# Kernel optimization log

Measured on AMD Instinct MI355X. Metric: run time of the kernel, lower is better.

The kernel has to match this reference:

```python
import jax, jax.numpy as jnp
import numpy as np

INPUT_DIM, HID_DIM, OUTPUT_DIM, N = 256, 128, 256, 16384
SCALE = 128 ** (-0.5)


def setup_inputs() -> dict:
    key = jax.random.key(0)
    ks = jax.random.split(key, 11)
    s_in = 1.0 / np.sqrt(INPUT_DIM)
    s_hid = 1.0 / np.sqrt(HID_DIM)
    return {
        "q": jax.random.normal(ks[0], (N, INPUT_DIM), jnp.float32),
        "k": jax.random.normal(ks[1], (N, INPUT_DIM), jnp.float32),
        "v": jax.random.normal(ks[2], (N, INPUT_DIM), jnp.float32),
        "Wq": jax.random.uniform(ks[3], (INPUT_DIM, HID_DIM), jnp.float32, -s_in, s_in),
        "bq": jax.random.uniform(ks[4], (HID_DIM,), jnp.float32, -s_in, s_in),
        "Wk": jax.random.uniform(ks[5], (INPUT_DIM, HID_DIM), jnp.float32, -s_in, s_in),
        "bk": jax.random.uniform(ks[6], (HID_DIM,), jnp.float32, -s_in, s_in),
        "Wv": jax.random.uniform(ks[7], (INPUT_DIM, HID_DIM), jnp.float32, -s_in, s_in),
        "bv": jax.random.uniform(ks[8], (HID_DIM,), jnp.float32, -s_in, s_in),
        "Wo": jax.random.uniform(ks[9], (HID_DIM, OUTPUT_DIM), jnp.float32, -s_hid, s_hid),
        "bo": jax.random.uniform(ks[10], (OUTPUT_DIM,), jnp.float32, -s_hid, s_hid),
    }


def reference(q, k, v, Wq, bq, Wk, bk, Wv, bv, Wo, bo):
    qh = q @ Wq + bq                      # [N, H]
    kh = k @ Wk + bk                      # [N, H]
    vh = v @ Wv + bv                      # [N, H]
    scores = (qh @ kh.T) * SCALE          # [N, N] materialized as in original
    attn = jax.nn.softmax(scores, axis=-1)
    out = attn @ vh                       # [N, H]
    return out @ Wo + bo                  # [N, OUTPUT_DIM]
```

## Files before the change

kernel.cpp:

```cpp
#include <hip/hip_runtime.h>
#include <hip/hip_bf16.h>
#include <stdint.h>


#define N_TOK 16384
#define IN_DIM 256
#define HID 128
#define OUT_DIM 256
#define KVB 32
#define BM 128
#define TOT_TILES (N_TOK / KVB)

typedef __bf16   bf16x8 __attribute__((ext_vector_type(8)));
typedef short    short8 __attribute__((ext_vector_type(8)));
typedef float    f32x4  __attribute__((ext_vector_type(4)));
typedef float    f32x16 __attribute__((ext_vector_type(16)));
typedef uint32_t u32x4  __attribute__((ext_vector_type(4)));

#define MFMA16(a,b,c) __builtin_amdgcn_mfma_f32_16x16x32_bf16((a),(b),(c),0,0,0)
#define MFMA32(a,b,c) __builtin_amdgcn_mfma_f32_32x32x16_bf16((a),(b),(c),0,0,0)
#define EXP2(x) __builtin_amdgcn_exp2f(x)

__device__ __forceinline__ short f2bf(float f) {
    union { float f; uint32_t u; } v; v.f = f;
    uint32_t r = v.u + 0x7FFFu + ((v.u >> 16) & 1u);
    return (short)(r >> 16);
}

__device__ __forceinline__ uint32_t cvtpk(float lo, float hi) {
    uint32_t d;
    asm("v_cvt_pk_bf16_f32 %0, %1, %2" : "=v"(d) : "v"(lo), "v"(hi));
    return d;
}

__device__ __forceinline__ void pswap(uint32_t& a, uint32_t& b) {
    auto r = __builtin_amdgcn_permlane32_swap(a, b, false, false);
    a = r[0]; b = r[1];
}

__device__ __forceinline__ void gl16(const void* g, const void* l) {
    __builtin_amdgcn_global_load_lds(
        (const __attribute__((address_space(1))) void*)g,
        (__attribute__((address_space(3))) void*)l, 16, 0, 0);
}

__global__ void wt4_kernel(const float* __restrict__ Wq, const float* __restrict__ Wk,
                           const float* __restrict__ Wv, const float* __restrict__ Wo,
                           short* __restrict__ tq, short* __restrict__ tk,
                           short* __restrict__ tv, short* __restrict__ to_)
{
    int idx = blockIdx.x * 256 + threadIdx.x;
    int w = idx >> 15, i = idx & 32767;
    if (w < 3) {
        const float* W = (w == 0) ? Wq : (w == 1) ? Wk : Wv;
        short* T = (w == 0) ? tq : (w == 1) ? tk : tv;
        int k = i >> 7, c = i & 127;
        T[c * 256 + k] = f2bf(W[i]);
    } else {
        int k = i >> 8, c = i & 255;
        to_[c * 128 + k] = f2bf(Wo[i]);
    }
}

__global__ __launch_bounds__(256) void proj3_kernel(
    const float* __restrict__ q, const float* __restrict__ k, const float* __restrict__ v,
    const short* __restrict__ tq, const short* __restrict__ tk, const short* __restrict__ tv,
    const float* __restrict__ bq, const float* __restrict__ bk, const float* __restrict__ bv,
    short* __restrict__ qh, short* __restrict__ kh, short* __restrict__ vh,
    float scale_q)
{
    const int y = blockIdx.y;
    const float* X  = (y == 0) ? q  : (y == 1) ? k  : v;
    const short* WT = (y == 0) ? tq : (y == 1) ? tk : tv;
    const float* bias = (y == 0) ? bq : (y == 1) ? bk : bv;
    short* Y = (y == 0) ? qh : (y == 1) ? kh : vh;
    const float post_scale = (y == 0) ? scale_q : 1.0f;

    const int lane = threadIdx.x & 63;
    const int wave = threadIdx.x >> 6;
    const int g = lane >> 4, c = lane & 15;
    const int rowbase = blockIdx.x * 64 + wave * 16;

    bf16x8 a[8];
    const float* xrow = X + (size_t)(rowbase + c) * IN_DIM;
#pragma unroll
    for (int kk = 0; kk < 8; ++kk) {
        const float* p = xrow + kk * 32 + 8 * g;
        float4 f0 = *(const float4*)(p);
        float4 f1 = *(const float4*)(p + 4);
        short8 t;
        t[0]=f2bf(f0.x); t[1]=f2bf(f0.y); t[2]=f2bf(f0.z); t[3]=f2bf(f0.w);
        t[4]=f2bf(f1.x); t[5]=f2bf(f1.y); t[6]=f2bf(f1.z); t[7]=f2bf(f1.w);
        a[kk] = __builtin_bit_cast(bf16x8, t);
    }

    f32x4 acc[8];
#pragma unroll
    for (int nf = 0; nf < 8; ++nf) acc[nf] = (f32x4){0.f, 0.f, 0.f, 0.f};

#pragma unroll
    for (int kk = 0; kk < 8; ++kk) {
#pragma unroll
        for (int nf = 0; nf < 8; ++nf) {
            bf16x8 b = *(const bf16x8*)(WT + (size_t)(c + 16 * nf) * IN_DIM + kk * 32 + 8 * g);
            acc[nf] = MFMA16(a[kk], b, acc[nf]);
        }
    }

#pragma unroll
    for (int nf = 0; nf < 8; ++nf) {
        int col = c + 16 * nf;
        float bval = bias[col];
#pragma unroll
        for (int r = 0; r < 4; ++r) {
            int row = rowbase + 4 * g + r;
            short val = f2bf((acc[nf][r] + bval) * post_scale);
            if (y == 0) {
                Y[(size_t)row * HID + col] = val;
            } else if (y == 1) {
                Y[(size_t)(row >> 5) * 4096 + (col >> 4) * 512 + ((col >> 3) & 1) * 256
                  + (row & 31) * 8 + (col & 7)] = val;
            } else {
                Y[(size_t)(row >> 5) * 4096 + ((row >> 4) & 1) * 2048 + (col >> 5) * 512
                  + ((row >> 3) & 1) * 256 + (col & 31) * 8 + (row & 7)] = val;
            }
        }
    }
}

__global__ __launch_bounds__(256, 3) void flash_kernel(
    const short* __restrict__ qh, const short* __restrict__ kh,
    const short* __restrict__ vh,
    short* __restrict__ Opart, float* __restrict__ Lpart,
    int nsplit)
{
    __shared__ short K_lds[3][KVB * HID];

    const int tid  = threadIdx.x;
    const int lane = tid & 63;
    const int wave = tid >> 6;
    const int hi   = lane >> 5;
    const int col  = lane & 31;

    const int lid = blockIdx.x;
    const int split = lid >> 7;
    const int qtile = lid & 127;

    const int qb = qtile * BM + wave * 32;
    const int tbase = TOT_TILES / nsplit, trem = TOT_TILES % nsplit;
    const int ntiles = tbase + (split < trem ? 1 : 0);
    const int ktile0 = tbase * split + (split < trem ? split : trem);

    bf16x8 qf[8];
    const short* qrow = qh + (size_t)(qb + col) * HID + 8 * hi;
#pragma unroll
    for (int kk = 0; kk < 8; ++kk)
        qf[kk] = *(const bf16x8*)(qrow + 16 * kk);

    f32x16 o[4];
#pragma unroll
    for (int nf = 0; nf < 4; ++nf)
#pragma unroll
        for (int i = 0; i < 16; ++i) o[nf][i] = 0.f;
    float l_run = 0.f;

    const short* kbase = kh + (size_t)ktile0 * 4096;
    const short* vbase = vh + (size_t)ktile0 * 4096;
    const int lds_off = tid * 8;
    const int frag_off = hi * 256 + col * 8;

    auto stageK = [&](int t, int buf) {
        const short* ks = kbase + (size_t)t * 4096 + lds_off;
        gl16(ks,        &K_lds[buf][lds_off]);
        gl16(ks + 2048, &K_lds[buf][2048 + lds_off]);
    };

    stageK(0, 0);
    stageK(1 < ntiles ? 1 : 0, 1);
    asm volatile("s_waitcnt vmcnt(2)" ::: "memory");
    __builtin_amdgcn_s_barrier();

    for (int t = 0; t < ntiles; ++t) {
        const int cur = t % 3;

        bf16x8 vf[8];
        {
            const short* vp = vbase + (size_t)t * 4096 + frag_off;
#pragma unroll
            for (int f = 0; f < 8; ++f)
                vf[f] = *(const bf16x8*)(vp + f * 512);
        }
        {
            const int tK = (t + 2 < ntiles) ? t + 2 : t;
            stageK(tK, (t + 2) % 3);
        }
        asm volatile("" ::: "memory");

        const short* Kc = &K_lds[cur][0];
        f32x16 s0;
#pragma unroll
        for (int i = 0; i < 16; ++i) s0[i] = 0.f;
        __builtin_amdgcn_s_setprio(1);
#pragma unroll
        for (int kk = 0; kk < 8; ++kk) {
            bf16x8 ka = *(const bf16x8*)(Kc + kk * 512 + frag_off);
            s0 = MFMA32(ka, qf[kk], s0);
        }
        __builtin_amdgcn_s_setprio(0);

        bf16x8 pa[2];
        {
            float e[16];
#pragma unroll
            for (int i = 0; i < 16; ++i) e[i] = EXP2(s0[i]);
            l_run += (((e[0]+e[1])+(e[2]+e[3])) + ((e[4]+e[5])+(e[6]+e[7])))
                   + (((e[8]+e[9])+(e[10]+e[11])) + ((e[12]+e[13])+(e[14]+e[15])));
            uint32_t x0 = cvtpk(e[0], e[1]),   x1 = cvtpk(e[2], e[3]);
            uint32_t x2 = cvtpk(e[4], e[5]),   x3 = cvtpk(e[6], e[7]);
            uint32_t x4 = cvtpk(e[8], e[9]),   x5 = cvtpk(e[10], e[11]);
            uint32_t x6 = cvtpk(e[12], e[13]), x7 = cvtpk(e[14], e[15]);
            pswap(x0, x2);  pswap(x1, x3);
            pswap(x4, x6);  pswap(x5, x7);
            u32x4 wA, wB;
            wA[0] = x0; wA[1] = x1; wA[2] = x2; wA[3] = x3;
            wB[0] = x4; wB[1] = x5; wB[2] = x6; wB[3] = x7;
            pa[0] = __builtin_bit_cast(bf16x8, wA);
            pa[1] = __builtin_bit_cast(bf16x8, wB);
        }

        asm volatile("s_waitcnt vmcnt(2)" ::: "memory");

        __builtin_amdgcn_s_setprio(1);
#pragma unroll
        for (int ks = 0; ks < 2; ++ks)
#pragma unroll
            for (int nf = 0; nf < 4; ++nf)
                o[nf] = MFMA32(pa[ks], vf[ks * 4 + nf], o[nf]);
        __builtin_amdgcn_s_setprio(0);

        __builtin_amdgcn_s_barrier();
    }

    {
        uint32_t ax = __builtin_bit_cast(uint32_t, l_run), bx = ax;
        pswap(ax, bx);
        l_run = __builtin_bit_cast(float, ax) + __builtin_bit_cast(float, bx);
    }
    const size_t sbase = (size_t)split * N_TOK + qb;
#pragma unroll
    for (int nf = 0; nf < 4; ++nf)
#pragma unroll
        for (int r = 0; r < 16; ++r) {
            int qr = (r & 3) + 8 * (r >> 2) + 4 * hi;
            Opart[(sbase + qr) * HID + 32 * nf + col] = f2bf(o[nf][r]);
        }
    if (lane < 32)
        Lpart[sbase + col] = l_run;
}

__global__ __launch_bounds__(256) void oproj_kernel(
    const short* __restrict__ Opart, const float* __restrict__ Lpart,
    const short* __restrict__ WoT, const float* __restrict__ bo,
    float* __restrict__ out, int nsplit)
{
    const int lane = threadIdx.x & 63;
    const int wave = threadIdx.x >> 6;
    const int g = lane >> 4, c = lane & 15;
    const int rowbase = blockIdx.x * 64 + wave * 16;
    const int row = rowbase + c;

    float denom = 0.f;
    for (int s = 0; s < nsplit; ++s) denom += Lpart[(size_t)s * N_TOK + row];
    const float inv = 1.0f / denom;

    float osum[4][8];
#pragma unroll
    for (int kk = 0; kk < 4; ++kk)
#pragma unroll
        for (int j = 0; j < 8; ++j) osum[kk][j] = 0.f;
    for (int s = 0; s < nsplit; ++s) {
        const short* orow = Opart + ((size_t)s * N_TOK + row) * HID;
#pragma unroll
        for (int kk = 0; kk < 4; ++kk) {
            bf16x8 vv = *(const bf16x8*)(orow + kk * 32 + 8 * g);
#pragma unroll
            for (int j = 0; j < 8; ++j) osum[kk][j] += (float)vv[j];
        }
    }
    bf16x8 a[4];
#pragma unroll
    for (int kk = 0; kk < 4; ++kk) {
        short8 t;
#pragma unroll
        for (int j = 0; j < 8; ++j) t[j] = f2bf(osum[kk][j] * inv);
        a[kk] = __builtin_bit_cast(bf16x8, t);
    }

    f32x4 acc[16];
#pragma unroll
    for (int nf = 0; nf < 16; ++nf) acc[nf] = (f32x4){0.f, 0.f, 0.f, 0.f};
#pragma unroll
    for (int kk = 0; kk < 4; ++kk)
#pragma unroll
        for (int nf = 0; nf < 16; ++nf) {
            bf16x8 b = *(const bf16x8*)(WoT + (size_t)(c + 16 * nf) * HID + kk * 32 + 8 * g);
            acc[nf] = MFMA16(a[kk], b, acc[nf]);
        }

#pragma unroll
    for (int nf = 0; nf < 16; ++nf) {
        int colo = c + 16 * nf;
        float bval = bo[colo];
#pragma unroll
        for (int r = 0; r < 4; ++r)
            out[(size_t)(rowbase + 4 * g + r) * OUT_DIM + colo] = acc[nf][r] + bval;
    }
}

extern "C" void kernel_launch(void* const* d_in, const int* in_sizes, int n_in,
                              void* d_out, int out_size, void* d_ws, size_t ws_size,
                              hipStream_t stream)
{
    (void)in_sizes; (void)n_in; (void)out_size;
    const float* q  = (const float*)d_in[0];
    const float* k  = (const float*)d_in[1];
    const float* v  = (const float*)d_in[2];
    const float* Wq = (const float*)d_in[3];
    const float* bq = (const float*)d_in[4];
    const float* Wk = (const float*)d_in[5];
    const float* bk = (const float*)d_in[6];
    const float* Wv = (const float*)d_in[7];
    const float* bvp= (const float*)d_in[8];
    const float* Wo = (const float*)d_in[9];
    const float* bo = (const float*)d_in[10];
    float* out = (float*)d_out;

    auto need = [](int ns) -> size_t {
        return (size_t)(4 * 65536)
             + (size_t)3 * N_TOK * HID * 2
             + (size_t)ns * N_TOK * HID * 2
             + (size_t)ns * N_TOK * 4
             + (size_t)64 * 1024;
    };
    int nsplit = 6;
    if (ws_size < need(6)) nsplit = 4;
    if (ws_size < need(4)) nsplit = 2;
    if (ws_size < need(2)) nsplit = 1;

    char* base = (char*)d_ws;
    size_t off = 0;
    auto alloc = [&](size_t bytes) -> void* {
        void* p = base + off;
        off = (off + bytes + 255) & ~(size_t)255;
        return p;
    };
    short* wtq = (short*)alloc(128 * 256 * 2);
    short* wtk = (short*)alloc(128 * 256 * 2);
    short* wtv = (short*)alloc(128 * 256 * 2);
    short* wto = (short*)alloc(256 * 128 * 2);
    short* qh  = (short*)alloc((size_t)N_TOK * HID * 2);
    short* khb = (short*)alloc((size_t)N_TOK * HID * 2);
    short* vhb = (short*)alloc((size_t)N_TOK * HID * 2);
    short* Opart = (short*)alloc((size_t)nsplit * N_TOK * HID * 2);
    float* Lp  = (float*)alloc((size_t)nsplit * N_TOK * 4);

    const float SCALE_L2E = 0.088388347648318447f * 1.4426950408889634f;

    wt4_kernel<<<512, 256, 0, stream>>>(Wq, Wk, Wv, Wo, wtq, wtk, wtv, wto);

    proj3_kernel<<<dim3(N_TOK / 64, 3), 256, 0, stream>>>(
        q, k, v, wtq, wtk, wtv, bq, bk, bvp, qh, khb, vhb, SCALE_L2E);

    flash_kernel<<<dim3(128 * nsplit), 256, 0, stream>>>(
        qh, khb, vhb, Opart, Lp, nsplit);

    oproj_kernel<<<N_TOK / 64, 256, 0, stream>>>(
        Opart, Lp, wto, bo, out, nsplit);
}
```

Measured before the change: 195.5 us.

## Double query rows per wave, stage V through LDS, and map splits to XCDs

```diff
diff --git a/kernel.cpp b/kernel.cpp
--- a/kernel.cpp
+++ b/kernel.cpp
@@ -8,7 +8,7 @@
 #define HID 128
 #define OUT_DIM 256
 #define KVB 32
-#define BM 128
+#define BM 256
 #define TOT_TILES (N_TOK / KVB)
 
 typedef __bf16   bf16x8 __attribute__((ext_vector_type(8)));
@@ -128,13 +128,14 @@
     }
 }
 
-__global__ __launch_bounds__(256, 3) void flash_kernel(
+__global__ __launch_bounds__(256, 2) void flash_kernel(
     const short* __restrict__ qh, const short* __restrict__ kh,
     const short* __restrict__ vh,
     short* __restrict__ Opart, float* __restrict__ Lpart,
     int nsplit)
 {
     __shared__ short K_lds[3][KVB * HID];
+    __shared__ short V_lds[3][KVB * HID];
 
     const int tid  = threadIdx.x;
     const int lane = tid & 63;
@@ -143,78 +144,77 @@
     const int col  = lane & 31;
 
     const int lid = blockIdx.x;
-    const int split = lid >> 7;
-    const int qtile = lid & 127;
-
-    const int qb = qtile * BM + wave * 32;
-    const int tbase = TOT_TILES / nsplit, trem = TOT_TILES % nsplit;
-    const int ntiles = tbase + (split < trem ? 1 : 0);
-    const int ktile0 = tbase * split + (split < trem ? split : trem);
-
-    bf16x8 qf[8];
-    const short* qrow = qh + (size_t)(qb + col) * HID + 8 * hi;
-#pragma unroll
-    for (int kk = 0; kk < 8; ++kk)
-        qf[kk] = *(const bf16x8*)(qrow + 16 * kk);
-
-    f32x16 o[4];
+    const int xcd = lid & 7;
+    const int split = xcd & (nsplit - 1);
+    const int qtile = (lid >> 3) * (8 / nsplit) + (xcd / nsplit);
+
+    const int qb = qtile * BM + wave * 64;
+    const int ntiles = TOT_TILES / nsplit;
+    const int ktile0 = split * ntiles;
+
+    bf16x8 qf0[8], qf1[8];
+    {
+        const short* qrow0 = qh + (size_t)(qb + col) * HID + 8 * hi;
+        const short* qrow1 = qh + (size_t)(qb + 32 + col) * HID + 8 * hi;
+#pragma unroll
+        for (int kk = 0; kk < 8; ++kk) {
+            qf0[kk] = *(const bf16x8*)(qrow0 + 16 * kk);
+            qf1[kk] = *(const bf16x8*)(qrow1 + 16 * kk);
+        }
+    }
+
+    f32x16 o0[4], o1[4];
 #pragma unroll
     for (int nf = 0; nf < 4; ++nf)
 #pragma unroll
-        for (int i = 0; i < 16; ++i) o[nf][i] = 0.f;
-    float l_run = 0.f;
+        for (int i = 0; i < 16; ++i) { o0[nf][i] = 0.f; o1[nf][i] = 0.f; }
+    float l0 = 0.f, l1 = 0.f;
 
     const short* kbase = kh + (size_t)ktile0 * 4096;
     const short* vbase = vh + (size_t)ktile0 * 4096;
     const int lds_off = tid * 8;
     const int frag_off = hi * 256 + col * 8;
 
-    auto stageK = [&](int t, int buf) {
+    auto stage = [&](int t, int buf) {
         const short* ks = kbase + (size_t)t * 4096 + lds_off;
+        const short* vs = vbase + (size_t)t * 4096 + lds_off;
         gl16(ks,        &K_lds[buf][lds_off]);
         gl16(ks + 2048, &K_lds[buf][2048 + lds_off]);
+        gl16(vs,        &V_lds[buf][lds_off]);
+        gl16(vs + 2048, &V_lds[buf][2048 + lds_off]);
     };
 
-    stageK(0, 0);
-    stageK(1 < ntiles ? 1 : 0, 1);
-    asm volatile("s_waitcnt vmcnt(2)" ::: "memory");
+    stage(0, 0);
+    stage(1 < ntiles ? 1 : 0, 1);
+    asm volatile("s_waitcnt vmcnt(4)" ::: "memory");
     __builtin_amdgcn_s_barrier();
 
     for (int t = 0; t < ntiles; ++t) {
         const int cur = t % 3;
-
-        bf16x8 vf[8];
         {
-            const short* vp = vbase + (size_t)t * 4096 + frag_off;
-#pragma unroll
-            for (int f = 0; f < 8; ++f)
-                vf[f] = *(const bf16x8*)(vp + f * 512);
-        }
+            const int tS = (t + 2 < ntiles) ? t + 2 : t;
+            stage(tS, (t + 2) % 3);
+        }
+        const short* Kc = &K_lds[cur][0];
+        const short* Vc = &V_lds[cur][0];
+
+        bf16x8 pa0[2], pa1[2];
         {
-            const int tK = (t + 2 < ntiles) ? t + 2 : t;
-            stageK(tK, (t + 2) % 3);
-        }
-        asm volatile("" ::: "memory");
-
-        const short* Kc = &K_lds[cur][0];
-        f32x16 s0;
-#pragma unroll
-        for (int i = 0; i < 16; ++i) s0[i] = 0.f;
-        __builtin_amdgcn_s_setprio(1);
-#pragma unroll
-        for (int kk = 0; kk < 8; ++kk) {
-            bf16x8 ka = *(const bf16x8*)(Kc + kk * 512 + frag_off);
-            s0 = MFMA32(ka, qf[kk], s0);
-        }
-        __builtin_amdgcn_s_setprio(0);
-
-        bf16x8 pa[2];
-        {
+            f32x16 s;
+#pragma unroll
+            for (int i = 0; i < 16; ++i) s[i] = 0.f;
+            __builtin_amdgcn_s_setprio(1);
+#pragma unroll
+            for (int kk = 0; kk < 8; ++kk) {
+                bf16x8 ka = *(const bf16x8*)(Kc + kk * 512 + frag_off);
+                s = MFMA32(ka, qf0[kk], s);
+            }
+            __builtin_amdgcn_s_setprio(0);
             float e[16];
 #pragma unroll
-            for (int i = 0; i < 16; ++i) e[i] = EXP2(s0[i]);
-            l_run += (((e[0]+e[1])+(e[2]+e[3])) + ((e[4]+e[5])+(e[6]+e[7])))
-                   + (((e[8]+e[9])+(e[10]+e[11])) + ((e[12]+e[13])+(e[14]+e[15])));
+            for (int i = 0; i < 16; ++i) e[i] = EXP2(s[i]);
+            l0 += (((e[0]+e[1])+(e[2]+e[3])) + ((e[4]+e[5])+(e[6]+e[7])))
+                + (((e[8]+e[9])+(e[10]+e[11])) + ((e[12]+e[13])+(e[14]+e[15])));
             uint32_t x0 = cvtpk(e[0], e[1]),   x1 = cvtpk(e[2], e[3]);
             uint32_t x2 = cvtpk(e[4], e[5]),   x3 = cvtpk(e[6], e[7]);
             uint32_t x4 = cvtpk(e[8], e[9]),   x5 = cvtpk(e[10], e[11]);
@@ -224,27 +224,60 @@
             u32x4 wA, wB;
             wA[0] = x0; wA[1] = x1; wA[2] = x2; wA[3] = x3;
             wB[0] = x4; wB[1] = x5; wB[2] = x6; wB[3] = x7;
-            pa[0] = __builtin_bit_cast(bf16x8, wA);
-            pa[1] = __builtin_bit_cast(bf16x8, wB);
-        }
-
-        asm volatile("s_waitcnt vmcnt(2)" ::: "memory");
+            pa0[0] = __builtin_bit_cast(bf16x8, wA);
+            pa0[1] = __builtin_bit_cast(bf16x8, wB);
+        }
+        {
+            f32x16 s;
+#pragma unroll
+            for (int i = 0; i < 16; ++i) s[i] = 0.f;
+            __builtin_amdgcn_s_setprio(1);
+#pragma unroll
+            for (int kk = 0; kk < 8; ++kk) {
+                bf16x8 ka = *(const bf16x8*)(Kc + kk * 512 + frag_off);
+                s = MFMA32(ka, qf1[kk], s);
+            }
+            __builtin_amdgcn_s_setprio(0);
+            float e[16];
+#pragma unroll
+            for (int i = 0; i < 16; ++i) e[i] = EXP2(s[i]);
+            l1 += (((e[0]+e[1])+(e[2]+e[3])) + ((e[4]+e[5])+(e[6]+e[7])))
+                + (((e[8]+e[9])+(e[10]+e[11])) + ((e[12]+e[13])+(e[14]+e[15])));
+            uint32_t x0 = cvtpk(e[0], e[1]),   x1 = cvtpk(e[2], e[3]);
+            uint32_t x2 = cvtpk(e[4], e[5]),   x3 = cvtpk(e[6], e[7]);
+            uint32_t x4 = cvtpk(e[8], e[9]),   x5 = cvtpk(e[10], e[11]);
+            uint32_t x6 = cvtpk(e[12], e[13]), x7 = cvtpk(e[14], e[15]);
+            pswap(x0, x2);  pswap(x1, x3);
+            pswap(x4, x6);  pswap(x5, x7);
+            u32x4 wA, wB;
+            wA[0] = x0; wA[1] = x1; wA[2] = x2; wA[3] = x3;
+            wB[0] = x4; wB[1] = x5; wB[2] = x6; wB[3] = x7;
+            pa1[0] = __builtin_bit_cast(bf16x8, wA);
+            pa1[1] = __builtin_bit_cast(bf16x8, wB);
+        }
 
         __builtin_amdgcn_s_setprio(1);
 #pragma unroll
         for (int ks = 0; ks < 2; ++ks)
 #pragma unroll
-            for (int nf = 0; nf < 4; ++nf)
-                o[nf] = MFMA32(pa[ks], vf[ks * 4 + nf], o[nf]);
+            for (int nf = 0; nf < 4; ++nf) {
+                bf16x8 vf = *(const bf16x8*)(Vc + ks * 2048 + nf * 512 + frag_off);
+                o0[nf] = MFMA32(pa0[ks], vf, o0[nf]);
+                o1[nf] = MFMA32(pa1[ks], vf, o1[nf]);
+            }
         __builtin_amdgcn_s_setprio(0);
 
+        asm volatile("s_waitcnt vmcnt(4)" ::: "memory");
         __builtin_amdgcn_s_barrier();
     }
 
     {
-        uint32_t ax = __builtin_bit_cast(uint32_t, l_run), bx = ax;
+        uint32_t ax = __builtin_bit_cast(uint32_t, l0), bx = ax;
         pswap(ax, bx);
-        l_run = __builtin_bit_cast(float, ax) + __builtin_bit_cast(float, bx);
+        l0 = __builtin_bit_cast(float, ax) + __builtin_bit_cast(float, bx);
+        uint32_t cx = __builtin_bit_cast(uint32_t, l1), dx = cx;
+        pswap(cx, dx);
+        l1 = __builtin_bit_cast(float, cx) + __builtin_bit_cast(float, dx);
     }
     const size_t sbase = (size_t)split * N_TOK + qb;
 #pragma unroll
@@ -252,10 +285,13 @@
 #pragma unroll
         for (int r = 0; r < 16; ++r) {
             int qr = (r & 3) + 8 * (r >> 2) + 4 * hi;
-            Opart[(sbase + qr) * HID + 32 * nf + col] = f2bf(o[nf][r]);
-        }
-    if (lane < 32)
-        Lpart[sbase + col] = l_run;
+            Opart[(sbase + qr) * HID + 32 * nf + col] = f2bf(o0[nf][r]);
+            Opart[(sbase + 32 + qr) * HID + 32 * nf + col] = f2bf(o1[nf][r]);
+        }
+    if (lane < 32) {
+        Lpart[sbase + col] = l0;
+        Lpart[sbase + 32 + col] = l1;
+    }
 }
 
 __global__ __launch_bounds__(256) void oproj_kernel(
@@ -342,8 +378,8 @@
              + (size_t)ns * N_TOK * 4
              + (size_t)64 * 1024;
     };
-    int nsplit = 6;
-    if (ws_size < need(6)) nsplit = 4;
+    int nsplit = 8;
+    if (ws_size < need(8)) nsplit = 4;
     if (ws_size < need(4)) nsplit = 2;
     if (ws_size < need(2)) nsplit = 1;
 
@@ -371,7 +407,7 @@
     proj3_kernel<<<dim3(N_TOK / 64, 3), 256, 0, stream>>>(
         q, k, v, wtq, wtk, wtv, bq, bk, bvp, qh, khb, vhb, SCALE_L2E);
 
-    flash_kernel<<<dim3(128 * nsplit), 256, 0, stream>>>(
+    flash_kernel<<<dim3((N_TOK / BM) * nsplit), 256, 0, stream>>>(
         qh, khb, vhb, Opart, Lp, nsplit);
 
     oproj_kernel<<<N_TOK / 64, 256, 0, stream>>>(
```

Result: slower. 202.8 us (+3.7%).

## Stage V tiles through LDS with triple-buffered async loads alongside K

Applied to the files above, without the earlier changes.

```diff
diff --git a/kernel.cpp b/kernel.cpp
--- a/kernel.cpp
+++ b/kernel.cpp
@@ -135,6 +135,7 @@
     int nsplit)
 {
     __shared__ short K_lds[3][KVB * HID];
+    __shared__ short V_lds[3][KVB * HID];
 
     const int tid  = threadIdx.x;
     const int lane = tid & 63;
@@ -169,34 +170,26 @@
     const int lds_off = tid * 8;
     const int frag_off = hi * 256 + col * 8;
 
-    auto stageK = [&](int t, int buf) {
+    auto stage = [&](int t, int buf) {
         const short* ks = kbase + (size_t)t * 4096 + lds_off;
+        const short* vs = vbase + (size_t)t * 4096 + lds_off;
         gl16(ks,        &K_lds[buf][lds_off]);
         gl16(ks + 2048, &K_lds[buf][2048 + lds_off]);
+        gl16(vs,        &V_lds[buf][lds_off]);
+        gl16(vs + 2048, &V_lds[buf][2048 + lds_off]);
     };
 
-    stageK(0, 0);
-    stageK(1 < ntiles ? 1 : 0, 1);
-    asm volatile("s_waitcnt vmcnt(2)" ::: "memory");
+    stage(0, 0);
+    if (1 < ntiles) stage(1, 1); else stage(0, 1);
+    asm volatile("s_waitcnt vmcnt(4)" ::: "memory");
     __builtin_amdgcn_s_barrier();
 
     for (int t = 0; t < ntiles; ++t) {
         const int cur = t % 3;
-
-        bf16x8 vf[8];
-        {
-            const short* vp = vbase + (size_t)t * 4096 + frag_off;
-#pragma unroll
-            for (int f = 0; f < 8; ++f)
-                vf[f] = *(const bf16x8*)(vp + f * 512);
-        }
-        {
-            const int tK = (t + 2 < ntiles) ? t + 2 : t;
-            stageK(tK, (t + 2) % 3);
-        }
-        asm volatile("" ::: "memory");
-
+        if (t + 2 < ntiles) stage(t + 2, (t + 2) % 3);
         const short* Kc = &K_lds[cur][0];
+        const short* Vc = &V_lds[cur][0];
+
         f32x16 s0;
 #pragma unroll
         for (int i = 0; i < 16; ++i) s0[i] = 0.f;
@@ -228,16 +221,19 @@
             pa[1] = __builtin_bit_cast(bf16x8, wB);
         }
 
-        asm volatile("s_waitcnt vmcnt(2)" ::: "memory");
-
         __builtin_amdgcn_s_setprio(1);
 #pragma unroll
         for (int ks = 0; ks < 2; ++ks)
 #pragma unroll
-            for (int nf = 0; nf < 4; ++nf)
-                o[nf] = MFMA32(pa[ks], vf[ks * 4 + nf], o[nf]);
+            for (int nf = 0; nf < 4; ++nf) {
+                bf16x8 vf = *(const bf16x8*)(Vc + ks * 2048 + nf * 512
+                                             + frag_off);
+                o[nf] = MFMA32(pa[ks], vf, o[nf]);
+            }
         __builtin_amdgcn_s_setprio(0);
 
+        if (t + 2 < ntiles)      asm volatile("s_waitcnt vmcnt(4)" ::: "memory");
+        else if (t + 1 < ntiles) asm volatile("s_waitcnt vmcnt(0)" ::: "memory");
         __builtin_amdgcn_s_barrier();
     }
 
```

Measured after the change: 183.8 us, median of 2. 1.06x faster.
